# Optimization experiments

Hardware: AMD Instinct MI355X
Metric: run time of the kernel (lower is better)

Reference implementation:

```python
import jax, jax.numpy as jnp
import numpy as np

B, L, H, E = 32, 256, 8, 16
SEQ_LEN = 64          # init seq_len, used only in final view
OUT = 256             # out_channels, must be divisible by SEQ_LEN
A = E + 1 + 128       # augmented channels: original + time + conv(128)
SIG_CH = A + A * A    # depth-2 signature channels
DN = ('NWC', 'WIO', 'NWC')


def setup_inputs() -> dict:
    key = jax.random.key(0)
    ks = jax.random.split(key, 8)
    return {
        'q': jax.random.normal(ks[0], (B, L, H, E), jnp.float32),
        'k': jax.random.normal(ks[1], (B, L, H, E), jnp.float32),
        'v': jax.random.normal(ks[2], (B, L, H, E), jnp.float32),
        'mask': jnp.zeros((B, L), jnp.bool_),
        'conv1_w': jax.random.normal(ks[3], (3, E, 64), jnp.float32) * 0.1,
        'conv1_b': jnp.zeros((64,), jnp.float32),
        'conv2_w': jax.random.normal(ks[4], (1, 64, 128), jnp.float32) * 0.1,
        'conv2_b': jnp.zeros((128,), jnp.float32),
        'lin_w': jax.random.normal(ks[5], (SIG_CH, OUT), jnp.float32) * 0.01,
        'lin_b': jnp.zeros((OUT,), jnp.float32),
    }


def _signature_depth2(p):
    # p: [N, S, C] piecewise-linear path. Returns [N, C + C*C].
    dx = p[:, 1:] - p[:, :-1]                       # [N, S-1, C]
    s1 = dx.sum(axis=1)                             # level 1
    cum_excl = jnp.cumsum(dx, axis=1) - dx          # sum of increments before t
    # level 2: sum_{s<t} dx_s (x) dx_t + 0.5 * dx_t (x) dx_t
    s2 = jnp.einsum('nti,ntj->nij', cum_excl + 0.5 * dx, dx)
    return jnp.concatenate([s1, s2.reshape(s2.shape[0], -1)], axis=-1)


def reference(q, k, v, mask, conv1_w, conv1_b, conv2_w, conv2_b, lin_w, lin_b):
    Bq, Lq, Hq, Eq = q.shape
    x = q.transpose(0, 2, 1, 3).reshape(Bq * Hq, Lq, Eq)   # [N, L, E]
    T = Lq - 3 + 1                                          # valid-conv length, kernel 3
    # Augment pieces
    trunc = x[:, 2:]                                        # [N, T, E]
    time = jnp.broadcast_to(jnp.linspace(0.0, 1.0, T, dtype=x.dtype)[None, :, None],
                            (Bq * Hq, T, 1))
    a = jax.lax.conv_general_dilated(x, conv1_w, (1,), 'VALID', dimension_numbers=DN) + conv1_b
    a = jax.nn.relu(jax.lax.conv_general_dilated(a, conv2_w, (1,), 'VALID', dimension_numbers=DN) + conv2_b)
    aug = jnp.concatenate([trunc, time, a], axis=2)         # [N, T, A]
    # lead-lag transform as written in source: interleave along time -> [N, 2T, A]
    lag = jnp.concatenate([aug[:, 1:], aug[:, -1:]], axis=1)
    ll = jnp.stack([aug, lag], axis=2).reshape(aug.shape[0], 2 * T, aug.shape[2])
    sig = _signature_depth2(ll)                             # [N, SIG_CH]
    out = sig @ lin_w + lin_b                               # [N, OUT]
    return out.reshape(Bq, Hq, SEQ_LEN, -1)
```

## Files before the change

### kernel.cpp

```cpp
#include <hip/hip_runtime.h>
#include <hip/hip_bf16.h>

#define Bq 32
#define Lq 256
#define Hq 8
#define Eq 16
#define Nn (Bq*Hq)
#define T 254
#define A 145
#define SIG_CH (A + A*A)
#define KP 21184
#define OUT 256

typedef __attribute__((ext_vector_type(8))) short short8;
typedef __attribute__((ext_vector_type(8))) unsigned short ushort8;
typedef __attribute__((ext_vector_type(4))) float floatx4;

static __device__ __forceinline__ unsigned short f2bf(float v) {
    unsigned int u = __float_as_uint(v);
    unsigned int r = (u + 0x7FFFu + ((u >> 16) & 1u)) >> 16;
    return (unsigned short)r;
}
static __device__ __forceinline__ float bf2f(unsigned short b) {
    return __uint_as_float(((unsigned int)b) << 16);
}

__global__ __launch_bounds__(256) void wsplit_kernel(
    const float* __restrict__ w1, const float* __restrict__ w2,
    unsigned short* __restrict__ w1im_hi, unsigned short* __restrict__ w1im_lo,
    unsigned short* __restrict__ w2t_hi,  unsigned short* __restrict__ w2t_lo)
{
    int idx = blockIdx.x*256 + threadIdx.x;
    if (idx < 4096) {
        int c = idx & 63, k = idx >> 6;
        float v = (k < 48) ? w1[k*64 + c] : 0.f;
        unsigned short hb = f2bf(v);
        w1im_hi[c*64 + k] = hb;
        w1im_lo[c*64 + k] = f2bf(v - bf2f(hb));
    } else {
        int j = idx - 4096;
        int c = j & 127, i = j >> 7;
        float v = w2[i*128 + c];
        unsigned short hb = f2bf(v);
        w2t_hi[c*64 + i] = hb;
        w2t_lo[c*64 + i] = f2bf(v - bf2f(hb));
    }
}

#define MDS 40
#define OS3 36
#define XIS 72

__global__ __launch_bounds__(256) void augsig_kernel(
    const float* __restrict__ q,
    const float* __restrict__ b1, const float* __restrict__ b2,
    const unsigned short* __restrict__ w1im_hi, const unsigned short* __restrict__ w1im_lo,
    const unsigned short* __restrict__ w2t_hi,  const unsigned short* __restrict__ w2t_lo,
    unsigned short* __restrict__ sig_hi, unsigned short* __restrict__ sig_lo)
{
    __shared__ __align__(16) unsigned short mdb[3*160*MDS];
    __shared__ __align__(16) float outs[A*OS3];
    __shared__ __align__(16) float xsc[36*16];
    __shared__ __align__(16) float b1s[64];
    __shared__ __align__(16) float b2s[128];

    unsigned short* Mh = mdb;
    unsigned short* Ml = mdb + 160*MDS;
    unsigned short* Dh = mdb + 2*160*MDS;
    unsigned short* ximh = mdb;
    unsigned short* ximl = mdb + 3456;
    unsigned short* a1h  = mdb + 6912;
    unsigned short* a1l  = mdb + 10368;

    const int tid = threadIdx.x;
    const int n = blockIdx.x;
    const int b = n >> 3, h = n & 7;

    const int lane = tid & 63;
    const int wv   = tid >> 6;
    const int frow = lane & 15;
    const int quad = lane >> 4;
    const int wm = wv & 1, wn = wv >> 1;

    if (tid < 64)  b1s[tid] = b1[tid];
    if (tid < 128) b2s[tid] = b2[tid];

    const float4* q4 = (const float4*)q + ((long)(b*Lq)*Hq + h)*4;
    const float inv253 = 1.0f / 253.0f;

    float a0 = 0.f, vlast = 0.f;

    floatx4 acc[5][5];
    #pragma unroll
    for (int i = 0; i < 5; ++i)
        #pragma unroll
        for (int j = 0; j < 5; ++j)
            acc[i][j] = (floatx4){0.f, 0.f, 0.f, 0.f};

    #pragma unroll 1
    for (int c = 0; c < 8; ++c) {
        const int t0 = c*32;

        if (tid < 140) {
            int r = tid >> 2, e4 = tid & 3;
            int t = t0 + r; if (t > 255) t = 255;
            *((float4*)xsc + (r*4 + e4)) = q4[t*32 + e4];
        }
        __syncthreads();

        for (int idx = tid; idx < 48*8; idx += 256) {
            int r = idx >> 3, g = idx & 7;
            unsigned short hh[8], ll[8];
            if (r <= 32 && g < 6) {
                const float* src = &xsc[r*16 + g*8];
                #pragma unroll
                for (int e = 0; e < 8; ++e) {
                    float v = src[e];
                    unsigned short hb = f2bf(v);
                    hh[e] = hb; ll[e] = f2bf(v - bf2f(hb));
                }
            } else {
                #pragma unroll
                for (int e = 0; e < 8; ++e) { hh[e] = 0; ll[e] = 0; }
            }
            *(ushort8*)&ximh[r*XIS + g*8] = *(ushort8*)hh;
            *(ushort8*)&ximl[r*XIS + g*8] = *(ushort8*)ll;
        }
        __syncthreads();

        {
            short8 ah[3][2], al[3][2];
            #pragma unroll
            for (int mt = 0; mt < 3; ++mt)
                #pragma unroll
                for (int ks = 0; ks < 2; ++ks) {
                    int ar = (mt*16 + frow)*XIS + ks*32 + quad*8;
                    ah[mt][ks] = *(const short8*)&ximh[ar];
                    al[mt][ks] = *(const short8*)&ximl[ar];
                }
            short8 bh[2], bl[2];
            #pragma unroll
            for (int ks = 0; ks < 2; ++ks) {
                int br = (wv*16 + frow)*64 + ks*32 + quad*8;
                bh[ks] = *(const short8*)(w1im_hi + br);
                bl[ks] = *(const short8*)(w1im_lo + br);
            }
            floatx4 acc1[3];
            #pragma unroll
            for (int mt = 0; mt < 3; ++mt) acc1[mt] = (floatx4){0.f,0.f,0.f,0.f};
            #pragma unroll
            for (int mt = 0; mt < 3; ++mt)
                #pragma unroll
                for (int ks = 0; ks < 2; ++ks) {
                    acc1[mt] = __builtin_amdgcn_mfma_f32_16x16x32_bf16(ah[mt][ks], bh[ks], acc1[mt], 0,0,0);
                    acc1[mt] = __builtin_amdgcn_mfma_f32_16x16x32_bf16(ah[mt][ks], bl[ks], acc1[mt], 0,0,0);
                    acc1[mt] = __builtin_amdgcn_mfma_f32_16x16x32_bf16(al[mt][ks], bh[ks], acc1[mt], 0,0,0);
                }
            const int cc = wv*16 + frow;
            const float bias = b1s[cc];
            #pragma unroll
            for (int mt = 0; mt < 3; ++mt)
                #pragma unroll
                for (int e = 0; e < 4; ++e) {
                    int t = mt*16 + quad*4 + e;
                    float v = acc1[mt][e] + bias;
                    unsigned short hb = f2bf(v);
                    a1h[t*XIS + cc] = hb;
                    a1l[t*XIS + cc] = f2bf(v - bf2f(hb));
                }
        }
        __syncthreads();

        {
            short8 ah[3][2], al[3][2];
            #pragma unroll
            for (int mt = 0; mt < 3; ++mt)
                #pragma unroll
                for (int ks = 0; ks < 2; ++ks) {
                    int ar = (mt*16 + frow)*XIS + ks*32 + quad*8;
                    ah[mt][ks] = *(const short8*)&a1h[ar];
                    al[mt][ks] = *(const short8*)&a1l[ar];
                }
            short8 bh[2][2], bl[2][2];
            #pragma unroll
            for (int nt = 0; nt < 2; ++nt)
                #pragma unroll
                for (int ks = 0; ks < 2; ++ks) {
                    int br = (wv*32 + nt*16 + frow)*64 + ks*32 + quad*8;
                    bh[nt][ks] = *(const short8*)(w2t_hi + br);
                    bl[nt][ks] = *(const short8*)(w2t_lo + br);
                }
            floatx4 acc2[3][2];
            #pragma unroll
            for (int mt = 0; mt < 3; ++mt)
                #pragma unroll
                for (int nt = 0; nt < 2; ++nt)
                    acc2[mt][nt] = (floatx4){0.f,0.f,0.f,0.f};
            #pragma unroll
            for (int mt = 0; mt < 3; ++mt)
                #pragma unroll
                for (int nt = 0; nt < 2; ++nt)
                    #pragma unroll
                    for (int ks = 0; ks < 2; ++ks) {
                        acc2[mt][nt] = __builtin_amdgcn_mfma_f32_16x16x32_bf16(ah[mt][ks], bh[nt][ks], acc2[mt][nt], 0,0,0);
                        acc2[mt][nt] = __builtin_amdgcn_mfma_f32_16x16x32_bf16(ah[mt][ks], bl[nt][ks], acc2[mt][nt], 0,0,0);
                        acc2[mt][nt] = __builtin_amdgcn_mfma_f32_16x16x32_bf16(al[mt][ks], bh[nt][ks], acc2[mt][nt], 0,0,0);
                    }
            #pragma unroll
            for (int mt = 0; mt < 3; ++mt)
                #pragma unroll
                for (int nt = 0; nt < 2; ++nt) {
                    int cc = wv*32 + nt*16 + frow;
                    float bias = b2s[cc];
                    int tb = mt*16 + quad*4;
                    if (tb <= 32) {
                        float4 vv;
                        vv.x = fmaxf(acc2[mt][nt][0] + bias, 0.f);
                        vv.y = fmaxf(acc2[mt][nt][1] + bias, 0.f);
                        vv.z = fmaxf(acc2[mt][nt][2] + bias, 0.f);
                        vv.w = fmaxf(acc2[mt][nt][3] + bias, 0.f);
                        *(float4*)&outs[(17 + cc)*OS3 + tb] = vv;
                    }
                }
        }
        for (int idx = tid; idx < 17*33; idx += 256) {
            int ch = idx / 33, tt = idx - ch*33;
            float val = (ch < 16) ? xsc[(tt+2)*16 + ch] : (float)(t0+tt)*inv253;
            outs[ch*OS3 + tt] = val;
        }
        __syncthreads();

        if (tid < 160) {
            unsigned short mh[32], ml[32], dh[32];
            if (tid < A) {
                float v[33];
                #pragma unroll
                for (int i = 0; i < 8; ++i)
                    *(float4*)&v[i*4] = *(const float4*)&outs[tid*OS3 + i*4];
                v[32] = outs[tid*OS3 + 32];
                if (c == 0) a0 = v[0];
                if (c == 7) vlast = v[29];
                #pragma unroll
                for (int tl = 0; tl < 32; ++tl) {
                    bool valid = (t0 + tl) <= 252;
                    float x0 = v[tl], x1 = v[tl+1];
                    float d = valid ? (x1 - x0) : 0.f;
                    float m = valid ? (0.5f*(x0 + x1) - a0) : 0.f;
                    unsigned short hb = f2bf(m);
                    mh[tl] = hb; ml[tl] = f2bf(m - bf2f(hb));
                    dh[tl] = f2bf(d);
                }
            } else {
                #pragma unroll
                for (int tl = 0; tl < 32; ++tl) { mh[tl]=0; ml[tl]=0; dh[tl]=0; }
            }
            #pragma unroll
            for (int pp = 0; pp < 4; ++pp) {
                *(ushort8*)&Mh[tid*MDS + pp*8] = *(ushort8*)&mh[pp*8];
                *(ushort8*)&Ml[tid*MDS + pp*8] = *(ushort8*)&ml[pp*8];
                *(ushort8*)&Dh[tid*MDS + pp*8] = *(ushort8*)&dh[pp*8];
            }
        }
        __syncthreads();

        {
            short8 afh[5], afl[5], bfh[5];
            #pragma unroll
            for (int i = 0; i < 5; ++i) {
                int ar = (wm*80 + i*16 + frow)*MDS + quad*8;
                int br = (wn*80 + i*16 + frow)*MDS + quad*8;
                afh[i] = *(const short8*)&Mh[ar];
                afl[i] = *(const short8*)&Ml[ar];
                bfh[i] = *(const short8*)&Dh[br];
            }
            #pragma unroll
            for (int mt = 0; mt < 5; ++mt)
                #pragma unroll
                for (int nt = 0; nt < 5; ++nt) {
                    acc[mt][nt] = __builtin_amdgcn_mfma_f32_16x16x32_bf16(
                        afh[mt], bfh[nt], acc[mt][nt], 0, 0, 0);
                    acc[mt][nt] = __builtin_amdgcn_mfma_f32_16x16x32_bf16(
                        afl[mt], bfh[nt], acc[mt][nt], 0, 0, 0);
                }
        }
    }

    unsigned short* sh = sig_hi + (long)n*KP;
    unsigned short* sl = sig_lo + (long)n*KP;
    if (tid < A) {
        float v = vlast - a0;
        unsigned short hb = f2bf(v);
        sh[tid] = hb;
        sl[tid] = f2bf(v - bf2f(hb));
    }
    if (tid >= 160 && tid < 160 + (KP - SIG_CH)) {
        sh[SIG_CH + tid - 160] = 0;
        sl[SIG_CH + tid - 160] = 0;
    }
    #pragma unroll
    for (int mt = 0; mt < 5; ++mt)
        #pragma unroll
        for (int nt = 0; nt < 5; ++nt) {
            int j = wn*80 + nt*16 + frow;
            int ib = wm*80 + mt*16 + quad*4;
            #pragma unroll
            for (int e = 0; e < 4; ++e) {
                int i = ib + e;
                if (i < A && j < A) {
                    float v = acc[mt][nt][e];
                    unsigned short hb = f2bf(v);
                    sh[A + i*A + j] = hb;
                    sl[A + i*A + j] = f2bf(v - bf2f(hb));
                }
            }
        }
}

__global__ __launch_bounds__(256) void wconv_kernel(
    const float* __restrict__ W,
    unsigned short* __restrict__ wt_hi, unsigned short* __restrict__ wt_lo)
{
    __shared__ float ls[64][65];
    const int tid = threadIdx.x;
    const int k0 = blockIdx.x * 64;
    const int o0 = blockIdx.y * 64;

    #pragma unroll
    for (int p = 0; p < 16; ++p) {
        int idx = tid + p*256;
        int kk = idx >> 6, oo = idx & 63;
        int k = k0 + kk;
        ls[kk][oo] = (k < SIG_CH) ? W[(long)k*OUT + o0 + oo] : 0.f;
    }
    __syncthreads();

    const int oo = tid >> 2;
    const int kq = (tid & 3) * 16;
    unsigned short hbuf[16], lbuf[16];
    #pragma unroll
    for (int j = 0; j < 16; ++j) {
        float v = ls[kq + j][oo];
        unsigned short hb = f2bf(v);
        hbuf[j] = hb;
        lbuf[j] = f2bf(v - bf2f(hb));
    }
    long off = (long)(o0 + oo)*KP + k0 + kq;
    *(ushort8*)(wt_hi + off)     = *(ushort8*)&hbuf[0];
    *(ushort8*)(wt_hi + off + 8) = *(ushort8*)&hbuf[8];
    *(ushort8*)(wt_lo + off)     = *(ushort8*)&lbuf[0];
    *(ushort8*)(wt_lo + off + 8) = *(ushort8*)&lbuf[8];
}

#define SPLITK 61
#define KC 352
#define NSTEP (KC/32)
#define LDA 40

__global__ __launch_bounds__(256) void gemm_kernel(
    const unsigned short* __restrict__ sig_hi, const unsigned short* __restrict__ sig_lo,
    const unsigned short* __restrict__ wt_hi,  const unsigned short* __restrict__ wt_lo,
    float* __restrict__ part)
{
    __shared__ __align__(16) unsigned short Ah[128*LDA];
    __shared__ __align__(16) unsigned short Al[128*LDA];
    __shared__ __align__(16) unsigned short Bh[128*LDA];
    __shared__ __align__(16) unsigned short Bl[128*LDA];

    const int tid = threadIdx.x;
    const int o0 = blockIdx.x * 128;
    const int n0 = blockIdx.y * 128;
    const int z  = blockIdx.z;
    const int k0 = z * KC;

    const int lane = tid & 63;
    const int w    = tid >> 6;
    const int wm   = w & 1;
    const int wn   = w >> 1;
    const int frow = lane & 15;
    const int quad = lane >> 4;

    const int srow = tid >> 1;
    const int kh   = (tid & 1) * 16;

    const unsigned short* gAh = sig_hi + (long)(n0 + srow)*KP;
    const unsigned short* gAl = sig_lo + (long)(n0 + srow)*KP;
    const unsigned short* gBh = wt_hi  + (long)(o0 + srow)*KP;
    const unsigned short* gBl = wt_lo  + (long)(o0 + srow)*KP;

    ushort8 rah[2], ral[2], rbh[2], rbl[2];
    const ushort8 z8 = {0,0,0,0,0,0,0,0};

    #define GLOAD(s)                                                          \
        {                                                                     \
            int kb = k0 + (s)*32 + kh;                                        \
            if (kb < KP) {                                                    \
                rah[0] = *(const ushort8*)(gAh + kb);                         \
                rah[1] = *(const ushort8*)(gAh + kb + 8);                     \
                ral[0] = *(const ushort8*)(gAl + kb);                         \
                ral[1] = *(const ushort8*)(gAl + kb + 8);                     \
                rbh[0] = *(const ushort8*)(gBh + kb);                         \
                rbh[1] = *(const ushort8*)(gBh + kb + 8);                     \
                rbl[0] = *(const ushort8*)(gBl + kb);                         \
                rbl[1] = *(const ushort8*)(gBl + kb + 8);                     \
            } else {                                                          \
                rah[0]=z8; rah[1]=z8; ral[0]=z8; ral[1]=z8;                   \
                rbh[0]=z8; rbh[1]=z8; rbl[0]=z8; rbl[1]=z8;                   \
            }                                                                 \
        }

    #define LSTORE()                                                          \
        {                                                                     \
            int o = srow*LDA + kh;                                            \
            *(ushort8*)(Ah + o)     = rah[0];                                 \
            *(ushort8*)(Ah + o + 8) = rah[1];                                 \
            *(ushort8*)(Al + o)     = ral[0];                                 \
            *(ushort8*)(Al + o + 8) = ral[1];                                 \
            *(ushort8*)(Bh + o)     = rbh[0];                                 \
            *(ushort8*)(Bh + o + 8) = rbh[1];                                 \
            *(ushort8*)(Bl + o)     = rbl[0];                                 \
            *(ushort8*)(Bl + o + 8) = rbl[1];                                 \
        }

    floatx4 acc[4][4];
    #pragma unroll
    for (int i = 0; i < 4; ++i)
        #pragma unroll
        for (int j = 0; j < 4; ++j)
            acc[i][j] = (floatx4){0.f, 0.f, 0.f, 0.f};

    GLOAD(0);
    LSTORE();
    __syncthreads();

    for (int s = 0; s < NSTEP; ++s) {
        if (s < NSTEP-1) GLOAD(s+1);

        short8 afh[4], afl[4], bfh[4], bfl[4];
        const int aoff = (wm*64 + frow)*LDA + quad*8;
        const int boff = (wn*64 + frow)*LDA + quad*8;
        #pragma unroll
        for (int tI = 0; tI < 4; ++tI) {
            afh[tI] = *(const short8*)(Ah + aoff + tI*16*LDA);
            afl[tI] = *(const short8*)(Al + aoff + tI*16*LDA);
            bfh[tI] = *(const short8*)(Bh + boff + tI*16*LDA);
            bfl[tI] = *(const short8*)(Bl + boff + tI*16*LDA);
        }
        #pragma unroll
        for (int mt = 0; mt < 4; ++mt)
            #pragma unroll
            for (int nt = 0; nt < 4; ++nt) {
                acc[mt][nt] = __builtin_amdgcn_mfma_f32_16x16x32_bf16(
                    afh[mt], bfh[nt], acc[mt][nt], 0, 0, 0);
                acc[mt][nt] = __builtin_amdgcn_mfma_f32_16x16x32_bf16(
                    afh[mt], bfl[nt], acc[mt][nt], 0, 0, 0);
                acc[mt][nt] = __builtin_amdgcn_mfma_f32_16x16x32_bf16(
                    afl[mt], bfh[nt], acc[mt][nt], 0, 0, 0);
            }
        __syncthreads();
        if (s < NSTEP-1) {
            LSTORE();
            __syncthreads();
        }
    }

    float* pz = part + (long)z * (Nn*OUT);
    #pragma unroll
    for (int mt = 0; mt < 4; ++mt)
        #pragma unroll
        for (int nt = 0; nt < 4; ++nt) {
            int col = o0 + wn*64 + nt*16 + frow;
            int rbase = n0 + wm*64 + mt*16 + quad*4;
            #pragma unroll
            for (int e = 0; e < 4; ++e)
                pz[(long)(rbase + e)*OUT + col] = acc[mt][nt][e];
        }
}

__global__ __launch_bounds__(256) void reduce_kernel(
    const float* __restrict__ part, const float* __restrict__ lb,
    float* __restrict__ out)
{
    int idx = blockIdx.x * 256 + threadIdx.x;
    float s = lb[idx & 255];
    #pragma unroll 8
    for (int z = 0; z < SPLITK; ++z)
        s += part[(long)z * (Nn*OUT) + idx];
    out[idx] = s;
}

extern "C" void kernel_launch(void* const* d_in, const int* in_sizes, int n_in,
                              void* d_out, int out_size, void* d_ws, size_t ws_size,
                              hipStream_t stream) {
    const float* q  = (const float*)d_in[0];
    const float* w1 = (const float*)d_in[4];
    const float* b1 = (const float*)d_in[5];
    const float* w2 = (const float*)d_in[6];
    const float* b2 = (const float*)d_in[7];
    const float* lw = (const float*)d_in[8];
    const float* lb = (const float*)d_in[9];
    float* out = (float*)d_out;

    char* ws = (char*)d_ws;
    unsigned short* sig_hi  = (unsigned short*)ws;
    unsigned short* sig_lo  = (unsigned short*)(ws + 10846208);
    unsigned short* wt_hi   = (unsigned short*)(ws + 21692416);
    unsigned short* wt_lo   = (unsigned short*)(ws + 32538624);
    float*          part    = (float*)(ws + 43384832);
    unsigned short* w1im_hi = (unsigned short*)(ws + 43384832);
    unsigned short* w1im_lo = (unsigned short*)(ws + 43384832 + 8192);
    unsigned short* w2t_hi  = (unsigned short*)(ws + 43384832 + 16384);
    unsigned short* w2t_lo  = (unsigned short*)(ws + 43384832 + 32768);

    wsplit_kernel<<<48, 256, 0, stream>>>(w1, w2, w1im_hi, w1im_lo, w2t_hi, w2t_lo);
    augsig_kernel<<<Nn, 256, 0, stream>>>(q, b1, b2, w1im_hi, w1im_lo, w2t_hi, w2t_lo, sig_hi, sig_lo);
    wconv_kernel<<<dim3(KP/64, OUT/64), 256, 0, stream>>>(lw, wt_hi, wt_lo);
    gemm_kernel<<<dim3(2, 2, SPLITK), 256, 0, stream>>>(sig_hi, sig_lo, wt_hi, wt_lo, part);
    reduce_kernel<<<(Nn*OUT)/256, 256, 0, stream>>>(part, lb, out);
}
```

Measured before the change: 170.9 us.

## Split augsig signature outer product across two blocks per sequence

Launches two blocks per (batch, head) sequence. Each block computes half of the row range of the A×A level-2 signature accumulator (3 row tiles instead of 5 per wave), while both recompute the conv front-end and the path increments. The conv weight fragments are also hoisted out of the time loop into registers. The aim is to double block count for better CU occupancy and to cut per-thread accumulator registers, at the cost of doing the conv/augmentation work twice.

```diff
diff --git a/kernel.cpp b/kernel.cpp
--- a/kernel.cpp
+++ b/kernel.cpp
@@ -73,7 +73,8 @@
     unsigned short* a1l  = mdb + 10368;
 
     const int tid = threadIdx.x;
-    const int n = blockIdx.x;
+    const int n = blockIdx.x >> 1;
+    const int hb2 = blockIdx.x & 1;
     const int b = n >> 3, h = n & 7;
 
     const int lane = tid & 63;
@@ -81,6 +82,8 @@
     const int frow = lane & 15;
     const int quad = lane >> 4;
     const int wm = wv & 1, wn = wv >> 1;
+    const int rb = hb2*64 + wm*48;
+    const int cb = wn*80;
 
     if (tid < 64)  b1s[tid] = b1[tid];
     if (tid < 128) b2s[tid] = b2[tid];
@@ -88,11 +91,28 @@
     const float4* q4 = (const float4*)q + ((long)(b*Lq)*Hq + h)*4;
     const float inv253 = 1.0f / 253.0f;
 
+    short8 c1bh[2], c1bl[2];
+    #pragma unroll
+    for (int ks = 0; ks < 2; ++ks) {
+        int br = (wv*16 + frow)*64 + ks*32 + quad*8;
+        c1bh[ks] = *(const short8*)(w1im_hi + br);
+        c1bl[ks] = *(const short8*)(w1im_lo + br);
+    }
+    short8 c2bh[2][2], c2bl[2][2];
+    #pragma unroll
+    for (int nt = 0; nt < 2; ++nt)
+        #pragma unroll
+        for (int ks = 0; ks < 2; ++ks) {
+            int br = (wv*32 + nt*16 + frow)*64 + ks*32 + quad*8;
+            c2bh[nt][ks] = *(const short8*)(w2t_hi + br);
+            c2bl[nt][ks] = *(const short8*)(w2t_lo + br);
+        }
+
     float a0 = 0.f, vlast = 0.f;
 
-    floatx4 acc[5][5];
-    #pragma unroll
-    for (int i = 0; i < 5; ++i)
+    floatx4 acc[3][5];
+    #pragma unroll
+    for (int i = 0; i < 3; ++i)
         #pragma unroll
         for (int j = 0; j < 5; ++j)
             acc[i][j] = (floatx4){0.f, 0.f, 0.f, 0.f};
@@ -116,8 +136,8 @@
                 #pragma unroll
                 for (int e = 0; e < 8; ++e) {
                     float v = src[e];
-                    unsigned short hb = f2bf(v);
-                    hh[e] = hb; ll[e] = f2bf(v - bf2f(hb));
+                    unsigned short hbv = f2bf(v);
+                    hh[e] = hbv; ll[e] = f2bf(v - bf2f(hbv));
                 }
             } else {
                 #pragma unroll
@@ -138,13 +158,6 @@
                     ah[mt][ks] = *(const short8*)&ximh[ar];
                     al[mt][ks] = *(const short8*)&ximl[ar];
                 }
-            short8 bh[2], bl[2];
-            #pragma unroll
-            for (int ks = 0; ks < 2; ++ks) {
-                int br = (wv*16 + frow)*64 + ks*32 + quad*8;
-                bh[ks] = *(const short8*)(w1im_hi + br);
-                bl[ks] = *(const short8*)(w1im_lo + br);
-            }
             floatx4 acc1[3];
             #pragma unroll
             for (int mt = 0; mt < 3; ++mt) acc1[mt] = (floatx4){0.f,0.f,0.f,0.f};
@@ -152,9 +165,9 @@
             for (int mt = 0; mt < 3; ++mt)
                 #pragma unroll
                 for (int ks = 0; ks < 2; ++ks) {
-                    acc1[mt] = __builtin_amdgcn_mfma_f32_16x16x32_bf16(ah[mt][ks], bh[ks], acc1[mt], 0,0,0);
-                    acc1[mt] = __builtin_amdgcn_mfma_f32_16x16x32_bf16(ah[mt][ks], bl[ks], acc1[mt], 0,0,0);
-                    acc1[mt] = __builtin_amdgcn_mfma_f32_16x16x32_bf16(al[mt][ks], bh[ks], acc1[mt], 0,0,0);
+                    acc1[mt] = __builtin_amdgcn_mfma_f32_16x16x32_bf16(ah[mt][ks], c1bh[ks], acc1[mt], 0,0,0);
+                    acc1[mt] = __builtin_amdgcn_mfma_f32_16x16x32_bf16(ah[mt][ks], c1bl[ks], acc1[mt], 0,0,0);
+                    acc1[mt] = __builtin_amdgcn_mfma_f32_16x16x32_bf16(al[mt][ks], c1bh[ks], acc1[mt], 0,0,0);
                 }
             const int cc = wv*16 + frow;
             const float bias = b1s[cc];
@@ -164,9 +177,9 @@
                 for (int e = 0; e < 4; ++e) {
                     int t = mt*16 + quad*4 + e;
                     float v = acc1[mt][e] + bias;
-                    unsigned short hb = f2bf(v);
-                    a1h[t*XIS + cc] = hb;
-                    a1l[t*XIS + cc] = f2bf(v - bf2f(hb));
+                    unsigned short hbv = f2bf(v);
+                    a1h[t*XIS + cc] = hbv;
+                    a1l[t*XIS + cc] = f2bf(v - bf2f(hbv));
                 }
         }
         __syncthreads();
@@ -181,15 +194,6 @@
                     ah[mt][ks] = *(const short8*)&a1h[ar];
                     al[mt][ks] = *(const short8*)&a1l[ar];
                 }
-            short8 bh[2][2], bl[2][2];
-            #pragma unroll
-            for (int nt = 0; nt < 2; ++nt)
-                #pragma unroll
-                for (int ks = 0; ks < 2; ++ks) {
-                    int br = (wv*32 + nt*16 + frow)*64 + ks*32 + quad*8;
-                    bh[nt][ks] = *(const short8*)(w2t_hi + br);
-                    bl[nt][ks] = *(const short8*)(w2t_lo + br);
-                }
             floatx4 acc2[3][2];
             #pragma unroll
             for (int mt = 0; mt < 3; ++mt)
@@ -202,9 +206,9 @@
                 for (int nt = 0; nt < 2; ++nt)
                     #pragma unroll
                     for (int ks = 0; ks < 2; ++ks) {
-                        acc2[mt][nt] = __builtin_amdgcn_mfma_f32_16x16x32_bf16(ah[mt][ks], bh[nt][ks], acc2[mt][nt], 0,0,0);
-                        acc2[mt][nt] = __builtin_amdgcn_mfma_f32_16x16x32_bf16(ah[mt][ks], bl[nt][ks], acc2[mt][nt], 0,0,0);
-                        acc2[mt][nt] = __builtin_amdgcn_mfma_f32_16x16x32_bf16(al[mt][ks], bh[nt][ks], acc2[mt][nt], 0,0,0);
+                        acc2[mt][nt] = __builtin_amdgcn_mfma_f32_16x16x32_bf16(ah[mt][ks], c2bh[nt][ks], acc2[mt][nt], 0,0,0);
+                        acc2[mt][nt] = __builtin_amdgcn_mfma_f32_16x16x32_bf16(ah[mt][ks], c2bl[nt][ks], acc2[mt][nt], 0,0,0);
+                        acc2[mt][nt] = __builtin_amdgcn_mfma_f32_16x16x32_bf16(al[mt][ks], c2bh[nt][ks], acc2[mt][nt], 0,0,0);
                     }
             #pragma unroll
             for (int mt = 0; mt < 3; ++mt)
@@ -246,8 +250,8 @@
                     float x0 = v[tl], x1 = v[tl+1];
                     float d = valid ? (x1 - x0) : 0.f;
                     float m = valid ? (0.5f*(x0 + x1) - a0) : 0.f;
-                    unsigned short hb = f2bf(m);
-                    mh[tl] = hb; ml[tl] = f2bf(m - bf2f(hb));
+                    unsigned short hbv = f2bf(m);
+                    mh[tl] = hbv; ml[tl] = f2bf(m - bf2f(hbv));
                     dh[tl] = f2bf(d);
                 }
             } else {
@@ -264,17 +268,20 @@
         __syncthreads();
 
         {
-            short8 afh[5], afl[5], bfh[5];
-            #pragma unroll
-            for (int i = 0; i < 5; ++i) {
-                int ar = (wm*80 + i*16 + frow)*MDS + quad*8;
-                int br = (wn*80 + i*16 + frow)*MDS + quad*8;
+            short8 afh[3], afl[3], bfh[5];
+            #pragma unroll
+            for (int i = 0; i < 3; ++i) {
+                int ar = (rb + i*16 + frow)*MDS + quad*8;
                 afh[i] = *(const short8*)&Mh[ar];
                 afl[i] = *(const short8*)&Ml[ar];
-                bfh[i] = *(const short8*)&Dh[br];
-            }
-            #pragma unroll
-            for (int mt = 0; mt < 5; ++mt)
+            }
+            #pragma unroll
+            for (int j = 0; j < 5; ++j) {
+                int br = (cb + j*16 + frow)*MDS + quad*8;
+                bfh[j] = *(const short8*)&Dh[br];
+            }
+            #pragma unroll
+            for (int mt = 0; mt < 3; ++mt)
                 #pragma unroll
                 for (int nt = 0; nt < 5; ++nt) {
                     acc[mt][nt] = __builtin_amdgcn_mfma_f32_16x16x32_bf16(
@@ -287,30 +294,32 @@
 
     unsigned short* sh = sig_hi + (long)n*KP;
     unsigned short* sl = sig_lo + (long)n*KP;
-    if (tid < A) {
-        float v = vlast - a0;
-        unsigned short hb = f2bf(v);
-        sh[tid] = hb;
-        sl[tid] = f2bf(v - bf2f(hb));
-    }
-    if (tid >= 160 && tid < 160 + (KP - SIG_CH)) {
-        sh[SIG_CH + tid - 160] = 0;
-        sl[SIG_CH + tid - 160] = 0;
-    }
-    #pragma unroll
-    for (int mt = 0; mt < 5; ++mt)
+    if (hb2 == 0) {
+        if (tid < A) {
+            float v = vlast - a0;
+            unsigned short hbv = f2bf(v);
+            sh[tid] = hbv;
+            sl[tid] = f2bf(v - bf2f(hbv));
+        }
+        if (tid >= 160 && tid < 160 + (KP - SIG_CH)) {
+            sh[SIG_CH + tid - 160] = 0;
+            sl[SIG_CH + tid - 160] = 0;
+        }
+    }
+    #pragma unroll
+    for (int mt = 0; mt < 3; ++mt)
         #pragma unroll
         for (int nt = 0; nt < 5; ++nt) {
-            int j = wn*80 + nt*16 + frow;
-            int ib = wm*80 + mt*16 + quad*4;
+            int j = cb + nt*16 + frow;
+            int ib = rb + mt*16 + quad*4;
             #pragma unroll
             for (int e = 0; e < 4; ++e) {
                 int i = ib + e;
                 if (i < A && j < A) {
                     float v = acc[mt][nt][e];
-                    unsigned short hb = f2bf(v);
-                    sh[A + i*A + j] = hb;
-                    sl[A + i*A + j] = f2bf(v - bf2f(hb));
+                    unsigned short hbv = f2bf(v);
+                    sh[A + i*A + j] = hbv;
+                    sl[A + i*A + j] = f2bf(v - bf2f(hbv));
                 }
             }
         }
@@ -512,7 +521,7 @@
     unsigned short* w2t_lo  = (unsigned short*)(ws + 43384832 + 32768);
 
     wsplit_kernel<<<48, 256, 0, stream>>>(w1, w2, w1im_hi, w1im_lo, w2t_hi, w2t_lo);
-    augsig_kernel<<<Nn, 256, 0, stream>>>(q, b1, b2, w1im_hi, w1im_lo, w2t_hi, w2t_lo, sig_hi, sig_lo);
+    augsig_kernel<<<Nn*2, 256, 0, stream>>>(q, b1, b2, w1im_hi, w1im_lo, w2t_hi, w2t_lo, sig_hi, sig_lo);
     wconv_kernel<<<dim3(KP/64, OUT/64), 256, 0, stream>>>(lw, wt_hi, wt_lo);
     gemm_kernel<<<dim3(2, 2, SPLITK), 256, 0, stream>>>(sig_hi, sig_lo, wt_hi, wt_lo, part);
     reduce_kernel<<<(Nn*OUT)/256, 256, 0, stream>>>(part, lb, out);
```

Result: slower. 207.3 us (+21.3%).
